# Optimization experiments

Hardware: AMD Instinct MI355X
Metric: run time of the kernel (lower is better)

The kernel has to match this reference:

```python
import jax, jax.numpy as jnp
import numpy as np

D_MODEL = 1024
NUM_HEADS = 16
D_HEAD = D_MODEL // NUM_HEADS


def setup_inputs() -> dict:
    key = jax.random.key(0)
    ks = jax.random.split(key, 9)
    B, L, E = 2, 2048, D_MODEL
    bound = 1.0 / np.sqrt(E)  # torch nn.Linear init range
    inp = {
        "query": jax.random.normal(ks[0], (B, L, E), dtype=jnp.float32),
        "key": jax.random.normal(ks[1], (B, L, E), dtype=jnp.float32),
        "value": jax.random.normal(ks[2], (B, L, E), dtype=jnp.float32),
        "wq": jax.random.uniform(ks[3], (E, E), jnp.float32, -bound, bound),
        "bq": jax.random.uniform(ks[4], (E,), jnp.float32, -bound, bound),
        "wk": jax.random.uniform(ks[5], (E, E), jnp.float32, -bound, bound),
        "bk": jax.random.uniform(ks[6], (E,), jnp.float32, -bound, bound),
        "wv": jax.random.uniform(ks[7], (E, E), jnp.float32, -bound, bound),
        "bv": jax.random.uniform(ks[8], (E,), jnp.float32, -bound, bound),
    }
    return inp


def reference(query, key, value, wq, bq, wk, bk, wv, bv):
    B, L, E = query.shape
    H, Dh = NUM_HEADS, D_HEAD
    scale = Dh ** 0.5
    # linear projections (torch Linear: x @ W.T + b)
    q = (query @ wq.T + bq).reshape(B, L, H, Dh).transpose(0, 2, 1, 3)  # bhld
    k = (key @ wk.T + bk).reshape(B, L, H, Dh).transpose(0, 2, 1, 3)
    v = (value @ wv.T + bv).reshape(B, L, H, Dh).transpose(0, 2, 1, 3)
    scores = jnp.einsum("bhld,bhsd->bhls", q, k) / scale
    attn = jax.nn.softmax(scores, axis=-1)  # dropout p=0 / eval: identity
    out = jnp.einsum("bhls,bhsd->bhld", attn, v)
    return out.transpose(0, 2, 1, 3).reshape(B, L, E)
```

## Files before the change

kernel.cpp:

```cpp
#include <hip/hip_runtime.h>
#include <hip/hip_bf16.h>


typedef __attribute__((ext_vector_type(8))) short short8;
typedef __attribute__((ext_vector_type(4))) short short4v;
typedef __attribute__((ext_vector_type(4))) float floatx4;

#define L_SEQ 2048
#define EMB 1024
#define NH 16
#define DH 64
#define QSCALE 0.18033688011112042f

__device__ __forceinline__ void gl16(const void* g, void* l) {
  __builtin_amdgcn_global_load_lds(
      (const __attribute__((address_space(1))) void*)g,
      (__attribute__((address_space(3))) void*)l, 16, 0, 0);
}

__global__ void cvt6_kernel(const float* __restrict__ s0, const float* __restrict__ s1,
                            const float* __restrict__ s2, const float* __restrict__ s3,
                            const float* __restrict__ s4, const float* __restrict__ s5,
                            __hip_bfloat16* __restrict__ d0, __hip_bfloat16* __restrict__ d1,
                            __hip_bfloat16* __restrict__ d2, __hip_bfloat16* __restrict__ d3,
                            __hip_bfloat16* __restrict__ d4, __hip_bfloat16* __restrict__ d5,
                            int nx8, int nw8) {
  const int t = blockIdx.y;
  const float* src = (t == 0) ? s0 : (t == 1) ? s1 : (t == 2) ? s2
                   : (t == 3) ? s3 : (t == 4) ? s4 : s5;
  __hip_bfloat16* dst = (t == 0) ? d0 : (t == 1) ? d1 : (t == 2) ? d2
                      : (t == 3) ? d3 : (t == 4) ? d4 : d5;
  const int n8 = (t < 3) ? nx8 : nw8;
  int i = blockIdx.x * blockDim.x + threadIdx.x;
  const int stride = gridDim.x * blockDim.x;
  for (; i < n8; i += stride) {
    const float4* s4p = (const float4*)src;
    float4 a = s4p[2 * i];
    float4 b = s4p[2 * i + 1];
    union { short8 v; __hip_bfloat16 h[8]; } u;
    u.h[0] = __float2bfloat16(a.x); u.h[1] = __float2bfloat16(a.y);
    u.h[2] = __float2bfloat16(a.z); u.h[3] = __float2bfloat16(a.w);
    u.h[4] = __float2bfloat16(b.x); u.h[5] = __float2bfloat16(b.y);
    u.h[6] = __float2bfloat16(b.z); u.h[7] = __float2bfloat16(b.w);
    *(short8*)(dst + 8 * i) = u.v;
  }
}

#define CPAD 136
__global__ __launch_bounds__(256) void proj_kernel(
    const __hip_bfloat16* __restrict__ xq, const __hip_bfloat16* __restrict__ xk,
    const __hip_bfloat16* __restrict__ xv,
    const __hip_bfloat16* __restrict__ wqb, const __hip_bfloat16* __restrict__ wkb,
    const __hip_bfloat16* __restrict__ wvb,
    const float* __restrict__ bq, const float* __restrict__ bk,
    const float* __restrict__ bv,
    __hip_bfloat16* __restrict__ Qb, __hip_bfloat16* __restrict__ Kb,
    __hip_bfloat16* __restrict__ Vt) {
  __shared__ __align__(16) __hip_bfloat16 lds[128 * CPAD];
  const int tid = threadIdx.x;
  const int bx = blockIdx.x;
  const int by = blockIdx.y;
  const int p = by >> 3;
  const int n0 = (by & 7) * 128;
  const int m0 = bx * 128;
  const __hip_bfloat16* X = (p == 0) ? xq : (p == 1) ? xk : xv;
  const __hip_bfloat16* W = (p == 0) ? wqb : (p == 1) ? wkb : wvb;
  const float* bias = (p == 0) ? bq : (p == 1) ? bk : bv;

  const int w = tid >> 6, ln = tid & 63;
  const int wm = w & 1, wn = w >> 1;
  const int quad = ln >> 4, lr = ln & 15;

  floatx4 acc[4][4];
#pragma unroll
  for (int i = 0; i < 4; ++i)
#pragma unroll
    for (int j = 0; j < 4; ++j) acc[i][j] = (floatx4){0.f, 0.f, 0.f, 0.f};

  const int srow = tid >> 3;
  const int scol = (((tid & 7) ^ ((tid >> 3) & 7)) * 8);

  for (int kt = 0; kt < 16; ++kt) {
    const int k0 = kt * 64;
#pragma unroll
    for (int i = 0; i < 4; ++i) {
      gl16(X + (size_t)(m0 + i * 32 + srow) * EMB + k0 + scol,
           lds + i * 2048 + tid * 8);
      gl16(W + (size_t)(n0 + i * 32 + srow) * EMB + k0 + scol,
           lds + 8192 + i * 2048 + tid * 8);
    }
    __syncthreads();
#pragma unroll
    for (int ks = 0; ks < 2; ++ks) {
      short8 af[4], bf[4];
#pragma unroll
      for (int mt = 0; mt < 4; ++mt)
        af[mt] = *(const short8*)(lds + (wm * 64 + mt * 16 + lr) * 64 +
                                  (((ks * 4 + quad) ^ (lr & 7)) * 8));
#pragma unroll
      for (int nt = 0; nt < 4; ++nt)
        bf[nt] = *(const short8*)(lds + 8192 + (wn * 64 + nt * 16 + lr) * 64 +
                                  (((ks * 4 + quad) ^ (lr & 7)) * 8));
#pragma unroll
      for (int mt = 0; mt < 4; ++mt)
#pragma unroll
        for (int nt = 0; nt < 4; ++nt)
          acc[mt][nt] = __builtin_amdgcn_mfma_f32_16x16x32_bf16(
              af[mt], bf[nt], acc[mt][nt], 0, 0, 0);
    }
    __syncthreads();
  }

  if (p == 2) {
#pragma unroll
    for (int nt = 0; nt < 4; ++nt) {
      const int nl = wn * 64 + nt * 16 + lr;
      const float bb = bias[n0 + nl];
#pragma unroll
      for (int mt = 0; mt < 4; ++mt) {
        union { short4v v; __hip_bfloat16 h4[4]; } u;
#pragma unroll
        for (int r = 0; r < 4; ++r) u.h4[r] = __float2bfloat16(acc[mt][nt][r] + bb);
        *(short4v*)(&lds[nl * CPAD + wm * 64 + mt * 16 + quad * 4]) = u.v;
      }
    }
  } else {
    const float scl = (p == 0) ? QSCALE : 1.0f;
#pragma unroll
    for (int nt = 0; nt < 4; ++nt) {
      const int nl = wn * 64 + nt * 16 + lr;
      const float bb = bias[n0 + nl];
#pragma unroll
      for (int mt = 0; mt < 4; ++mt)
#pragma unroll
        for (int r = 0; r < 4; ++r)
          lds[(wm * 64 + mt * 16 + quad * 4 + r) * CPAD + nl] =
              __float2bfloat16((acc[mt][nt][r] + bb) * scl);
    }
  }
  __syncthreads();

  {
    const int tr = tid >> 1, half = tid & 1;
    const int b = m0 >> 11;
    const __hip_bfloat16* src = lds + tr * CPAD + half * 64;
    __hip_bfloat16* g;
    if (p == 2) {
      const int ng = n0 + tr;
      const int h = ng >> 6, d = ng & 63;
      g = Vt + ((size_t)((b * NH + h) * DH + d)) * L_SEQ + (m0 & 2047) + half * 64;
    } else {
      __hip_bfloat16* dst = (p == 0) ? Qb : Kb;
      const int m = m0 + tr;
      const int h = (n0 >> 6) + half;
      g = dst + ((size_t)((b * NH + h) * L_SEQ + (m & 2047))) * DH;
    }
#pragma unroll
    for (int j = 0; j < 8; ++j)
      *(short8*)(g + j * 8) = *(const short8*)(src + j * 8);
  }
}

__global__ __launch_bounds__(256, 4) void attn_kernel(
    const __hip_bfloat16* __restrict__ Qb, const __hip_bfloat16* __restrict__ Kb,
    const __hip_bfloat16* __restrict__ Vt, float* __restrict__ out,
    float* __restrict__ psP) {
  __shared__ __align__(16) __hip_bfloat16 Kl[2][4096];
  __shared__ __align__(16) __hip_bfloat16 Vl[2][4096];
  __shared__ __align__(16) __hip_bfloat16 Pl[4][2048];

  const int tid = threadIdx.x;
  const int w = tid >> 6, ln = tid & 63;
  const int quad = ln >> 4, lr = ln & 15;
  const int bh = blockIdx.y;
  const int sh = blockIdx.z;
  const int sbase = sh * 1024;
  const int q0 = blockIdx.x * 128 + w * 32;
  const __hip_bfloat16* Qp = Qb + (size_t)bh * L_SEQ * DH;
  const __hip_bfloat16* Kp = Kb + (size_t)bh * L_SEQ * DH;
  const __hip_bfloat16* Vp = Vt + (size_t)bh * DH * L_SEQ;

  short8 qf[2][2];
#pragma unroll
  for (int qs = 0; qs < 2; ++qs)
#pragma unroll
    for (int kk = 0; kk < 2; ++kk)
      qf[qs][kk] = *(const short8*)(Qp + (size_t)(q0 + qs * 16 + lr) * DH + kk * 32 + quad * 8);

  int koff[2], voff[2], loff[2];
#pragma unroll
  for (int i = 0; i < 2; ++i) {
    const int idx = i * 256 + tid;
    const int srow = idx >> 3;
    const int c = (idx & 7) ^ (srow & 7);
    koff[i] = srow * DH + c * 8;
    voff[i] = srow * L_SEQ + c * 8;
    loff[i] = idx * 8;
  }

  floatx4 acc[2][4];
  float psum[2];
#pragma unroll
  for (int qs = 0; qs < 2; ++qs) {
    psum[qs] = 0.f;
#pragma unroll
    for (int nt = 0; nt < 4; ++nt) acc[qs][nt] = (floatx4){0.f, 0.f, 0.f, 0.f};
  }

#pragma unroll
  for (int i = 0; i < 2; ++i) gl16(Kp + (size_t)sbase * DH + koff[i], &Kl[0][loff[i]]);
#pragma unroll
  for (int i = 0; i < 2; ++i) gl16(Vp + sbase + voff[i], &Vl[0][loff[i]]);

  const int xsw = lr & 7;
  const int xswp = (lr & 7) ^ ((lr >> 3) << 2);

  for (int it = 0; it < 16; ++it) {
    __syncthreads();
    if (it + 1 < 16) {
      const int s0 = sbase + (it + 1) * 64;
      const int bf = (it + 1) & 1;
#pragma unroll
      for (int i = 0; i < 2; ++i) gl16(Kp + (size_t)s0 * DH + koff[i], &Kl[bf][loff[i]]);
#pragma unroll
      for (int i = 0; i < 2; ++i) gl16(Vp + s0 + voff[i], &Vl[bf][loff[i]]);
    }
    const __hip_bfloat16* Kt = Kl[it & 1];
    const __hip_bfloat16* Vtile = Vl[it & 1];

#pragma unroll
    for (int mt = 0; mt < 4; ++mt) {
      floatx4 sc[2];
#pragma unroll
      for (int qs = 0; qs < 2; ++qs) sc[qs] = (floatx4){0.f, 0.f, 0.f, 0.f};
#pragma unroll
      for (int kk = 0; kk < 2; ++kk) {
        const short8 kf = *(const short8*)(Kt + ((mt * 16 + lr) * 8 + ((kk * 4 + quad) ^ xsw)) * 8);
#pragma unroll
        for (int qs = 0; qs < 2; ++qs)
          sc[qs] = __builtin_amdgcn_mfma_f32_16x16x32_bf16(kf, qf[qs][kk], sc[qs], 0, 0, 0);
      }
      const int cch = mt * 2 + (quad >> 1);
#pragma unroll
      for (int qs = 0; qs < 2; ++qs) {
        union { short4v v; __hip_bfloat16 h4[4]; } u;
#pragma unroll
        for (int r = 0; r < 4; ++r) {
          const float pv = __builtin_amdgcn_exp2f(sc[qs][r]);
          psum[qs] += pv;
          u.h4[r] = __float2bfloat16(pv);
        }
        const int row = qs * 16 + lr;
        *(short4v*)(&Pl[w][row * 64 + ((cch ^ xswp) * 8 + (quad & 1) * 4)]) = u.v;
      }
    }

#pragma unroll
    for (int kk = 0; kk < 2; ++kk) {
      short8 vf[4];
#pragma unroll
      for (int nt = 0; nt < 4; ++nt)
        vf[nt] = *(const short8*)(Vtile + ((nt * 16 + lr) * 8 + ((kk * 4 + quad) ^ xsw)) * 8);
#pragma unroll
      for (int qs = 0; qs < 2; ++qs) {
        const short8 pf = *(const short8*)(&Pl[w][(qs * 16 + lr) * 64 + ((kk * 4 + quad) ^ xswp) * 8]);
#pragma unroll
        for (int nt = 0; nt < 4; ++nt)
          acc[qs][nt] = __builtin_amdgcn_mfma_f32_16x16x32_bf16(pf, vf[nt], acc[qs][nt], 0, 0, 0);
      }
    }
  }

#pragma unroll
  for (int qs = 0; qs < 2; ++qs) {
    psum[qs] += __shfl_xor(psum[qs], 16, 64);
    psum[qs] += __shfl_xor(psum[qs], 32, 64);
  }

  if (quad == 0) {
#pragma unroll
    for (int qs = 0; qs < 2; ++qs)
      psP[sh * (32 * L_SEQ) + bh * L_SEQ + q0 + qs * 16 + lr] = psum[qs];
  }

  const int b = bh >> 4, h = bh & 15;
#pragma unroll
  for (int qs = 0; qs < 2; ++qs) {
#pragma unroll
    for (int r = 0; r < 4; ++r) {
      const int lq = q0 + qs * 16 + quad * 4 + r;
#pragma unroll
      for (int nt = 0; nt < 4; ++nt)
        atomicAdd(&out[((size_t)(b * L_SEQ + lq)) * EMB + h * DH + nt * 16 + lr],
                  acc[qs][nt][r]);
    }
  }
}

__global__ __launch_bounds__(256) void norm_kernel(float* __restrict__ out,
                                                   const float* __restrict__ psP) {
  const int idx4 = blockIdx.x * blockDim.x + threadIdx.x;
  const int flat = idx4 * 4;
  const int e = flat & 1023;
  const int l = (flat >> 10) & 2047;
  const int b = flat >> 21;
  const int bh = b * NH + (e >> 6);
  const float ps = psP[bh * L_SEQ + l] + psP[32 * L_SEQ + bh * L_SEQ + l];
  const float inv = 1.0f / ps;
  float4 v = ((float4*)out)[idx4];
  v.x *= inv; v.y *= inv; v.z *= inv; v.w *= inv;
  ((float4*)out)[idx4] = v;
}

extern "C" void kernel_launch(void* const* d_in, const int* in_sizes, int n_in,
                              void* d_out, int out_size, void* d_ws, size_t ws_size,
                              hipStream_t stream) {
  const float* xq = (const float*)d_in[0];
  const float* xk = (const float*)d_in[1];
  const float* xv = (const float*)d_in[2];
  const float* wq = (const float*)d_in[3];
  const float* bq = (const float*)d_in[4];
  const float* wk = (const float*)d_in[5];
  const float* bk = (const float*)d_in[6];
  const float* wv = (const float*)d_in[7];
  const float* bv = (const float*)d_in[8];

  const size_t NX = (size_t)4096 * 1024;
  const size_t NW = (size_t)1024 * 1024;
  __hip_bfloat16* xbq = (__hip_bfloat16*)d_ws;
  __hip_bfloat16* xbk = xbq + NX;
  __hip_bfloat16* xbv = xbk + NX;
  __hip_bfloat16* wbq = xbv + NX;
  __hip_bfloat16* wbk = wbq + NW;
  __hip_bfloat16* wbv = wbk + NW;
  __hip_bfloat16* Qb = wbv + NW;
  __hip_bfloat16* Kb = Qb + NX;
  __hip_bfloat16* Vt = Kb + NX;
  float* psP = (float*)xbv;

  hipMemsetAsync(d_out, 0, (size_t)out_size * sizeof(float), stream);

  cvt6_kernel<<<dim3(1024, 6), 256, 0, stream>>>(xq, xk, xv, wq, wk, wv,
                                                 xbq, xbk, xbv, wbq, wbk, wbv,
                                                 (int)(NX / 8), (int)(NW / 8));

  proj_kernel<<<dim3(32, 24), 256, 0, stream>>>(xbq, xbk, xbv, wbq, wbk, wbv,
                                                bq, bk, bv, Qb, Kb, Vt);
  attn_kernel<<<dim3(16, 32, 2), 256, 0, stream>>>(Qb, Kb, Vt, (float*)d_out, psP);
  norm_kernel<<<4096, 256, 0, stream>>>((float*)d_out, psP);
}
```

Before: 221.3 us.

## Double per-wave query rows and replace output atomics with bf16 split partials

Each wave now handles 64 query rows instead of 32, so every K/V tile loaded into shared memory is reused across twice as many queries and the grid halves. The float atomicAdd accumulation into the output, along with its memset, is replaced by plain bf16 stores of the two key-split partial results into workspace buffers. The normalization kernel then sums the two partials and divides by the softmax denominator. This trades more registers and LDS per block, and therefore lower occupancy, plus bf16 rounding of the partials, for less K/V traffic and no atomics.

```diff
diff --git a/kernel.cpp b/kernel.cpp
--- a/kernel.cpp
+++ b/kernel.cpp
@@ -161,13 +161,14 @@
   }
 }
 
-__global__ __launch_bounds__(256, 4) void attn_kernel(
+__global__ __launch_bounds__(256, 2) void attn_kernel(
     const __hip_bfloat16* __restrict__ Qb, const __hip_bfloat16* __restrict__ Kb,
-    const __hip_bfloat16* __restrict__ Vt, float* __restrict__ out,
+    const __hip_bfloat16* __restrict__ Vt,
+    __hip_bfloat16* __restrict__ Op0, __hip_bfloat16* __restrict__ Op1,
     float* __restrict__ psP) {
   __shared__ __align__(16) __hip_bfloat16 Kl[2][4096];
   __shared__ __align__(16) __hip_bfloat16 Vl[2][4096];
-  __shared__ __align__(16) __hip_bfloat16 Pl[4][2048];
+  __shared__ __align__(16) __hip_bfloat16 Pl[4][4096];
 
   const int tid = threadIdx.x;
   const int w = tid >> 6, ln = tid & 63;
@@ -175,14 +176,15 @@
   const int bh = blockIdx.y;
   const int sh = blockIdx.z;
   const int sbase = sh * 1024;
-  const int q0 = blockIdx.x * 128 + w * 32;
+  const int q0 = blockIdx.x * 256 + w * 64;
   const __hip_bfloat16* Qp = Qb + (size_t)bh * L_SEQ * DH;
   const __hip_bfloat16* Kp = Kb + (size_t)bh * L_SEQ * DH;
   const __hip_bfloat16* Vp = Vt + (size_t)bh * DH * L_SEQ;
-
-  short8 qf[2][2];
-#pragma unroll
-  for (int qs = 0; qs < 2; ++qs)
+  __hip_bfloat16* Op = sh ? Op1 : Op0;
+
+  short8 qf[4][2];
+#pragma unroll
+  for (int qs = 0; qs < 4; ++qs)
 #pragma unroll
     for (int kk = 0; kk < 2; ++kk)
       qf[qs][kk] = *(const short8*)(Qp + (size_t)(q0 + qs * 16 + lr) * DH + kk * 32 + quad * 8);
@@ -198,10 +200,10 @@
     loff[i] = idx * 8;
   }
 
-  floatx4 acc[2][4];
-  float psum[2];
-#pragma unroll
-  for (int qs = 0; qs < 2; ++qs) {
+  floatx4 acc[4][4];
+  float psum[4];
+#pragma unroll
+  for (int qs = 0; qs < 4; ++qs) {
     psum[qs] = 0.f;
 #pragma unroll
     for (int nt = 0; nt < 4; ++nt) acc[qs][nt] = (floatx4){0.f, 0.f, 0.f, 0.f};
@@ -230,19 +232,19 @@
 
 #pragma unroll
     for (int mt = 0; mt < 4; ++mt) {
-      floatx4 sc[2];
-#pragma unroll
-      for (int qs = 0; qs < 2; ++qs) sc[qs] = (floatx4){0.f, 0.f, 0.f, 0.f};
+      floatx4 sc[4];
+#pragma unroll
+      for (int qs = 0; qs < 4; ++qs) sc[qs] = (floatx4){0.f, 0.f, 0.f, 0.f};
 #pragma unroll
       for (int kk = 0; kk < 2; ++kk) {
         const short8 kf = *(const short8*)(Kt + ((mt * 16 + lr) * 8 + ((kk * 4 + quad) ^ xsw)) * 8);
 #pragma unroll
-        for (int qs = 0; qs < 2; ++qs)
+        for (int qs = 0; qs < 4; ++qs)
           sc[qs] = __builtin_amdgcn_mfma_f32_16x16x32_bf16(kf, qf[qs][kk], sc[qs], 0, 0, 0);
       }
       const int cch = mt * 2 + (quad >> 1);
 #pragma unroll
-      for (int qs = 0; qs < 2; ++qs) {
+      for (int qs = 0; qs < 4; ++qs) {
         union { short4v v; __hip_bfloat16 h4[4]; } u;
 #pragma unroll
         for (int r = 0; r < 4; ++r) {
@@ -262,7 +264,7 @@
       for (int nt = 0; nt < 4; ++nt)
         vf[nt] = *(const short8*)(Vtile + ((nt * 16 + lr) * 8 + ((kk * 4 + quad) ^ xsw)) * 8);
 #pragma unroll
-      for (int qs = 0; qs < 2; ++qs) {
+      for (int qs = 0; qs < 4; ++qs) {
         const short8 pf = *(const short8*)(&Pl[w][(qs * 16 + lr) * 64 + ((kk * 4 + quad) ^ xswp) * 8]);
 #pragma unroll
         for (int nt = 0; nt < 4; ++nt)
@@ -272,43 +274,51 @@
   }
 
 #pragma unroll
-  for (int qs = 0; qs < 2; ++qs) {
+  for (int qs = 0; qs < 4; ++qs) {
     psum[qs] += __shfl_xor(psum[qs], 16, 64);
     psum[qs] += __shfl_xor(psum[qs], 32, 64);
   }
-
   if (quad == 0) {
 #pragma unroll
-    for (int qs = 0; qs < 2; ++qs)
+    for (int qs = 0; qs < 4; ++qs)
       psP[sh * (32 * L_SEQ) + bh * L_SEQ + q0 + qs * 16 + lr] = psum[qs];
   }
 
-  const int b = bh >> 4, h = bh & 15;
-#pragma unroll
-  for (int qs = 0; qs < 2; ++qs) {
+#pragma unroll
+  for (int qs = 0; qs < 4; ++qs) {
 #pragma unroll
     for (int r = 0; r < 4; ++r) {
       const int lq = q0 + qs * 16 + quad * 4 + r;
+      __hip_bfloat16* dst = Op + ((size_t)(bh * L_SEQ + lq)) * DH;
 #pragma unroll
       for (int nt = 0; nt < 4; ++nt)
-        atomicAdd(&out[((size_t)(b * L_SEQ + lq)) * EMB + h * DH + nt * 16 + lr],
-                  acc[qs][nt][r]);
+        dst[nt * 16 + lr] = __float2bfloat16(acc[qs][nt][r]);
     }
   }
 }
 
 __global__ __launch_bounds__(256) void norm_kernel(float* __restrict__ out,
+                                                   const __hip_bfloat16* __restrict__ Op0,
+                                                   const __hip_bfloat16* __restrict__ Op1,
                                                    const float* __restrict__ psP) {
   const int idx4 = blockIdx.x * blockDim.x + threadIdx.x;
   const int flat = idx4 * 4;
   const int e = flat & 1023;
   const int l = (flat >> 10) & 2047;
   const int b = flat >> 21;
-  const int bh = b * NH + (e >> 6);
+  const int h = e >> 6, d = e & 63;
+  const int bh = b * NH + h;
   const float ps = psP[bh * L_SEQ + l] + psP[32 * L_SEQ + bh * L_SEQ + l];
   const float inv = 1.0f / ps;
-  float4 v = ((float4*)out)[idx4];
-  v.x *= inv; v.y *= inv; v.z *= inv; v.w *= inv;
+  const size_t src = ((size_t)(bh * L_SEQ + l)) * DH + d;
+  union { short4v v; __hip_bfloat16 h4[4]; } a, c;
+  a.v = *(const short4v*)(Op0 + src);
+  c.v = *(const short4v*)(Op1 + src);
+  float4 v;
+  v.x = (__bfloat162float(a.h4[0]) + __bfloat162float(c.h4[0])) * inv;
+  v.y = (__bfloat162float(a.h4[1]) + __bfloat162float(c.h4[1])) * inv;
+  v.z = (__bfloat162float(a.h4[2]) + __bfloat162float(c.h4[2])) * inv;
+  v.w = (__bfloat162float(a.h4[3]) + __bfloat162float(c.h4[3])) * inv;
   ((float4*)out)[idx4] = v;
 }
 
@@ -336,9 +346,9 @@
   __hip_bfloat16* Qb = wbv + NW;
   __hip_bfloat16* Kb = Qb + NX;
   __hip_bfloat16* Vt = Kb + NX;
-  float* psP = (float*)xbv;
-
-  hipMemsetAsync(d_out, 0, (size_t)out_size * sizeof(float), stream);
+  __hip_bfloat16* Op0 = xbq;
+  __hip_bfloat16* Op1 = xbk;
+  float* psP = (float*)wbq;
 
   cvt6_kernel<<<dim3(1024, 6), 256, 0, stream>>>(xq, xk, xv, wq, wk, wv,
                                                  xbq, xbk, xbv, wbq, wbk, wbv,
@@ -346,6 +356,6 @@
 
   proj_kernel<<<dim3(32, 24), 256, 0, stream>>>(xbq, xbk, xbv, wbq, wbk, wbv,
                                                 bq, bk, bv, Qb, Kb, Vt);
-  attn_kernel<<<dim3(16, 32, 2), 256, 0, stream>>>(Qb, Kb, Vt, (float*)d_out, psP);
-  norm_kernel<<<4096, 256, 0, stream>>>((float*)d_out, psP);
-}
+  attn_kernel<<<dim3(8, 32, 2), 256, 0, stream>>>(Qb, Kb, Vt, Op0, Op1, psP);
+  norm_kernel<<<4096, 256, 0, stream>>>((float*)d_out, Op0, Op1, psP);
+}
```

Measured after the change: 194.8 us. -12.0%, faster.
